# Kernel optimization log

Hardware: AMD Instinct MI355X
Metric: run time of the kernel (lower is better)

## Reference

```python
import jax, jax.numpy as jnp
import numpy as np

N = 2_097_152
TABLE = 32768  # hash table size (power of 2 -> mod == & 32767)
FEAT = 16
H = 64


def setup_inputs() -> dict:
    key = jax.random.key(0)
    k = jax.random.split(key, 9)
    pos = jax.random.normal(k[0], (N, 3), dtype=jnp.float32)
    normal = jax.random.normal(k[1], (N, 3), dtype=jnp.float32)
    emb = jax.random.normal(k[2], (TABLE, FEAT), dtype=jnp.float32) * 0.05
    W1 = jax.random.normal(k[3], (FEAT + 3, H), dtype=jnp.float32) * 0.1
    b1 = jnp.zeros((H,), jnp.float32)
    W2 = jax.random.normal(k[4], (H, H), dtype=jnp.float32) * 0.1
    b2 = jnp.zeros((H,), jnp.float32)
    W3 = jax.random.normal(k[5], (H, 3), dtype=jnp.float32) * 0.1
    b3 = jnp.zeros((3,), jnp.float32)
    return {"pos": pos, "normal": normal, "emb": emb,
            "W1": W1, "b1": b1, "W2": W2, "b2": b2, "W3": W3, "b3": b3}


def _hash_idx(pos):
    # torch .long() truncates toward zero; astype(int32) does the same.
    # Products only matter mod 2^15, so int32 wraparound is safe.
    s = (pos * 8.0).astype(jnp.int32)
    h = (s[:, 0] * np.int32(73856093)) ^ (s[:, 1] * np.int32(19349663)) ^ (s[:, 2] * np.int32(83492791))
    return h & np.int32(TABLE - 1)  # floor-mod by 2^15 == bitwise AND


def reference(pos, normal, emb, W1, b1, W2, b2, W3, b3):
    idx = _hash_idx(pos)                    # [N] int32
    feat = emb[idx]                         # [N,16] gather
    x = jnp.concatenate([feat, normal], axis=-1)  # [N,19]
    h1 = jax.nn.relu(x @ W1 + b1)           # [N,64]
    h2 = jax.nn.relu(h1 @ W2 + b2)          # [N,64]
    return jax.nn.sigmoid(h2 @ W3 + b3)     # [N,3]
```

## Files before the change

kernel.cpp:

```cpp
#include <hip/hip_runtime.h>
#include <cstdint>


typedef short  bf16x8 __attribute__((ext_vector_type(8)));
typedef float  f32x4  __attribute__((ext_vector_type(4)));

#define MFMA16(A, B, C) __builtin_amdgcn_mfma_f32_16x16x32_bf16((A), (B), (C), 0, 0, 0)

__device__ inline uint32_t f2b_u(float f) {
    union { float f; uint32_t u; } x; x.f = f;
    return (x.u + 0x7FFFu + ((x.u >> 16) & 1u)) >> 16;
}
__device__ inline short f2b(float f) { return (short)f2b_u(f); }

#if defined(__has_builtin)
#  if __has_builtin(__builtin_amdgcn_cvt_pk_bf16_f32)
#    define HAVE_PK_BF16 1
#  endif
#endif

__device__ inline int pk(float a, float b) {
#ifdef HAVE_PK_BF16
    auto v = __builtin_amdgcn_cvt_pk_bf16_f32(a, b);
    int i; __builtin_memcpy(&i, &v, sizeof(i));
    return i;
#else
    return (int)(f2b_u(a) | (f2b_u(b) << 16));
#endif
}

__device__ inline void cfence() { __asm__ volatile("" ::: "memory"); }

__device__ inline float sigmoid_fast(float x) {
    float e = __expf(-x);
    return __builtin_amdgcn_rcpf(1.0f + e);
}

#define XS 40
#define HS 72

__global__ __launch_bounds__(256, 3) void nrad_mfma_kernel(
    const float* __restrict__ pos, const float* __restrict__ nrm,
    const float* __restrict__ emb,
    const float* __restrict__ W1, const float* __restrict__ b1,
    const float* __restrict__ W2, const float* __restrict__ b2,
    const float* __restrict__ W3, const float* __restrict__ b3,
    float* __restrict__ out, int ntiles)
{
    __shared__ alignas(16) char arena[29696];
    short* w1t = (short*)arena;
    short* w2t = (short*)(arena + 4096);
    short* w3t = (short*)(arena + 12288);
    float* b2s = (float*)(arena + 12672);
    float* b3s = (float*)(arena + 12928);

    const int tid  = threadIdx.x;
    const int wave = tid >> 6;
    const int lane = tid & 63;
    const int q    = lane >> 4;
    const int nn   = lane & 15;

    for (int e = tid; e < 64 * 32; e += 256) {
        int n = e >> 5, k = e & 31;
        float v = (k < 19) ? W1[k * 64 + n] : (k == 19 ? b1[n] : 0.0f);
        w1t[n * 32 + k] = f2b(v);
    }
    for (int e = tid; e < 4096; e += 256) {
        int k = e >> 6, n = e & 63;
        w2t[n * 64 + k] = f2b(W2[e]);
    }
    for (int e = tid; e < 192; e += 256) {
        int k = e / 3, c = e - k * 3;
        w3t[c * 64 + k] = f2b(W3[e]);
    }
    for (int e = tid; e < 64; e += 256) b2s[e] = b2[e];
    if (tid < 4) b3s[tid] = (tid < 3) ? b3[tid] : 0.0f;
    __syncthreads();

    bf16x8 w1f[4], w2f[4][2], w3f[2];
    #pragma unroll
    for (int t = 0; t < 4; ++t)
        w1f[t] = *(const bf16x8*)(w1t + (t * 16 + nn) * 32 + q * 8);
    #pragma unroll
    for (int t = 0; t < 4; ++t)
        #pragma unroll
        for (int ks = 0; ks < 2; ++ks)
            w2f[t][ks] = *(const bf16x8*)(w2t + (t * 16 + nn) * 64 + ks * 32 + q * 8);
    {
        int c3 = (nn < 3) ? nn : 0;
        w3f[0] = *(const bf16x8*)(w3t + c3 * 64 + q * 8);
        w3f[1] = *(const bf16x8*)(w3t + c3 * 64 + 32 + q * 8);
    }
    f32x4 b2rv[4];
    #pragma unroll
    for (int t = 0; t < 4; ++t)
        b2rv[t] = *(const f32x4*)(b2s + t * 16 + q * 4);
    const float b3r = (nn < 3) ? b3s[nn] : 0.0f;
    __syncthreads();

    short* xw = (short*)(arena + wave * 5120);
    short* hw = (short*)(arena + 20480 + wave * 2304);

    const int xro  = nn * XS + q * 8;
    const int hro0 = nn * HS + q * 8;
    const int oofs = q * 12 + nn;

    const int wave_gid = blockIdx.x * 4 + wave;
    const int nwaves   = gridDim.x * 4;
    const float4* emb4 = (const float4*)emb;

    for (int tile = wave_gid; tile < ntiles; tile += nwaves) {
        const int base = tile * 64;
        const int i    = base + lane;

        const float* pp = pos + 3 * i;
        const float* np = nrm + 3 * i;
        float p0 = pp[0], p1 = pp[1], p2 = pp[2];
        float n0 = np[0], n1 = np[1], n2 = np[2];
        int s0 = (int)(p0 * 8.0f), s1 = (int)(p1 * 8.0f), s2 = (int)(p2 * 8.0f);
        uint32_t h = ((uint32_t)s0 * 73856093u) ^ ((uint32_t)s1 * 19349663u) ^
                     ((uint32_t)s2 * 83492791u);
        uint32_t idx = h & 32767u;
        float4 f0 = emb4[idx*4+0], f1 = emb4[idx*4+1];
        float4 f2 = emb4[idx*4+2], f3 = emb4[idx*4+3];

        int4 A = make_int4(pk(f0.x, f0.y), pk(f0.z, f0.w), pk(f1.x, f1.y), pk(f1.z, f1.w));
        int4 B = make_int4(pk(f2.x, f2.y), pk(f2.z, f2.w), pk(f3.x, f3.y), pk(f3.z, f3.w));
        int4 C = make_int4(pk(n0, n1), pk(n2, 1.0f), 0, 0);
        int4 D = make_int4(0, 0, 0, 0);
        int4* xr = (int4*)(xw + lane * XS);
        xr[0] = A; xr[1] = B; xr[2] = C; xr[3] = D;
        cfence();

        const float* ob = out + (size_t)base * 3;

        #pragma unroll
        for (int sub = 0; sub < 4; ++sub) {
            bf16x8 xf = *(const bf16x8*)(xw + sub * 16 * XS + xro);
            f32x4 acc1[4];
            #pragma unroll
            for (int t = 0; t < 4; ++t) {
                f32x4 z = {0.0f, 0.0f, 0.0f, 0.0f};
                acc1[t] = MFMA16(w1f[t], xf, z);
            }
            cfence();
            #pragma unroll
            for (int t = 0; t < 4; ++t) {
                float a0 = fmaxf(acc1[t][0], 0.0f), a1 = fmaxf(acc1[t][1], 0.0f);
                float a2 = fmaxf(acc1[t][2], 0.0f), a3 = fmaxf(acc1[t][3], 0.0f);
                *(int2*)(hw + nn * HS + t * 16 + q * 4) = make_int2(pk(a0, a1), pk(a2, a3));
            }
            cfence();

            bf16x8 h1f0 = *(const bf16x8*)(hw + hro0);
            bf16x8 h1f1 = *(const bf16x8*)(hw + hro0 + 32);
            f32x4 acc2[4];
            #pragma unroll
            for (int t = 0; t < 4; ++t) {
                f32x4 c2 = b2rv[t];
                c2 = MFMA16(w2f[t][0], h1f0, c2);
                acc2[t] = MFMA16(w2f[t][1], h1f1, c2);
            }
            cfence();
            #pragma unroll
            for (int t = 0; t < 4; ++t) {
                float a0 = fmaxf(acc2[t][0], 0.0f), a1 = fmaxf(acc2[t][1], 0.0f);
                float a2 = fmaxf(acc2[t][2], 0.0f), a3 = fmaxf(acc2[t][3], 0.0f);
                *(int2*)(hw + nn * HS + t * 16 + q * 4) = make_int2(pk(a0, a1), pk(a2, a3));
            }
            cfence();

            bf16x8 h2f0 = *(const bf16x8*)(hw + hro0);
            bf16x8 h2f1 = *(const bf16x8*)(hw + hro0 + 32);
            f32x4 acc3 = {b3r, b3r, b3r, b3r};
            acc3 = MFMA16(h2f0, w3f[0], acc3);
            acc3 = MFMA16(h2f1, w3f[1], acc3);
            cfence();

            float o0 = sigmoid_fast(acc3[0]);
            float o1 = sigmoid_fast(acc3[1]);
            float o2 = sigmoid_fast(acc3[2]);
            float o3 = sigmoid_fast(acc3[3]);
            if (nn < 3) {
                const float* dummy = ob;  (void)dummy;
                float* o = (float*)(ob + sub * 48 + oofs);
                o[0] = o0; o[3] = o1; o[6] = o2; o[9] = o3;
            }
        }
        cfence();
    }
}

extern "C" void kernel_launch(void* const* d_in, const int* in_sizes, int n_in,
                              void* d_out, int out_size, void* d_ws, size_t ws_size,
                              hipStream_t stream) {
    const float* pos = (const float*)d_in[0];
    const float* nrm = (const float*)d_in[1];
    const float* emb = (const float*)d_in[2];
    const float* W1  = (const float*)d_in[3];
    const float* b1  = (const float*)d_in[4];
    const float* W2  = (const float*)d_in[5];
    const float* b2  = (const float*)d_in[6];
    const float* W3  = (const float*)d_in[7];
    const float* b3  = (const float*)d_in[8];
    float* out = (float*)d_out;

    int n = in_sizes[0] / 3;
    int ntiles = n / 64;
    int grid = 1024;
    nrad_mfma_kernel<<<grid, 256, 0, stream>>>(pos, nrm, emb, W1, b1, W2, b2,
                                               W3, b3, out, ntiles);
}
```

Baseline: 165.8 us.

## Convert MFMA outputs to next-layer operands with permlane swaps instead of LDS

Replaces the per-layer LDS round trip (store the packed bf16 activations, then reload them as B-operand fragments) with in-register packing followed by v_permlane32_swap and v_permlane16_swap, which move the accumulator layout into the operand layout directly. This drops the hw LDS scratch, shrinking shared memory to 20 KB, and raises launch bounds to four blocks per CU. It also forces the inline-asm v_cvt_pk_bf16_f32 packing path. The risks are the correctness of the lane-permutation mapping and extra register pressure under the tighter occupancy bound.

```diff
diff --git a/kernel.cpp b/kernel.cpp
--- a/kernel.cpp
+++ b/kernel.cpp
@@ -7,26 +7,22 @@
 
 #define MFMA16(A, B, C) __builtin_amdgcn_mfma_f32_16x16x32_bf16((A), (B), (C), 0, 0, 0)
 
+__device__ inline int pk(float a, float b) {
+    int d;
+    __asm__("v_cvt_pk_bf16_f32 %0, %1, %2" : "=v"(d) : "v"(a), "v"(b));
+    return d;
+}
 __device__ inline uint32_t f2b_u(float f) {
     union { float f; uint32_t u; } x; x.f = f;
     return (x.u + 0x7FFFu + ((x.u >> 16) & 1u)) >> 16;
 }
 __device__ inline short f2b(float f) { return (short)f2b_u(f); }
 
-#if defined(__has_builtin)
-#  if __has_builtin(__builtin_amdgcn_cvt_pk_bf16_f32)
-#    define HAVE_PK_BF16 1
-#  endif
-#endif
-
-__device__ inline int pk(float a, float b) {
-#ifdef HAVE_PK_BF16
-    auto v = __builtin_amdgcn_cvt_pk_bf16_f32(a, b);
-    int i; __builtin_memcpy(&i, &v, sizeof(i));
-    return i;
-#else
-    return (int)(f2b_u(a) | (f2b_u(b) << 16));
-#endif
+__device__ inline void pl32_swap(int& a, int& b) {
+    __asm__ volatile("v_permlane32_swap_b32 %0, %1" : "+v"(a), "+v"(b));
+}
+__device__ inline void pl16_swap(int& a, int& b) {
+    __asm__ volatile("v_permlane16_swap_b32 %0, %1" : "+v"(a), "+v"(b));
 }
 
 __device__ inline void cfence() { __asm__ volatile("" ::: "memory"); }
@@ -36,10 +32,30 @@
     return __builtin_amdgcn_rcpf(1.0f + e);
 }
 
+__device__ inline void cd_to_frag(const f32x4 acc[4], int4& lo, int4& hi) {
+    int P0 = pk(fmaxf(acc[0][0],0.f), fmaxf(acc[0][1],0.f));
+    int P1 = pk(fmaxf(acc[0][2],0.f), fmaxf(acc[0][3],0.f));
+    int P2 = pk(fmaxf(acc[1][0],0.f), fmaxf(acc[1][1],0.f));
+    int P3 = pk(fmaxf(acc[1][2],0.f), fmaxf(acc[1][3],0.f));
+    int P4 = pk(fmaxf(acc[2][0],0.f), fmaxf(acc[2][1],0.f));
+    int P5 = pk(fmaxf(acc[2][2],0.f), fmaxf(acc[2][3],0.f));
+    int P6 = pk(fmaxf(acc[3][0],0.f), fmaxf(acc[3][1],0.f));
+    int P7 = pk(fmaxf(acc[3][2],0.f), fmaxf(acc[3][3],0.f));
+    pl32_swap(P0, P2); pl16_swap(P0, P2);
+    pl32_swap(P1, P3); pl16_swap(P1, P3);
+    pl32_swap(P4, P6); pl16_swap(P4, P6);
+    pl32_swap(P5, P7); pl16_swap(P5, P7);
+    lo = make_int4(P0, P1, P2, P3);
+    hi = make_int4(P4, P5, P6, P7);
+}
+
+__device__ inline bf16x8 as_frag(int4 v) {
+    bf16x8 f; __builtin_memcpy(&f, &v, sizeof(f)); return f;
+}
+
 #define XS 40
-#define HS 72
-
-__global__ __launch_bounds__(256, 3) void nrad_mfma_kernel(
+
+__global__ __launch_bounds__(256, 4) void nrad_mfma_kernel(
     const float* __restrict__ pos, const float* __restrict__ nrm,
     const float* __restrict__ emb,
     const float* __restrict__ W1, const float* __restrict__ b1,
@@ -47,7 +63,7 @@
     const float* __restrict__ W3, const float* __restrict__ b3,
     float* __restrict__ out, int ntiles)
 {
-    __shared__ alignas(16) char arena[29696];
+    __shared__ alignas(16) char arena[20480];
     short* w1t = (short*)arena;
     short* w2t = (short*)(arena + 4096);
     short* w3t = (short*)(arena + 12288);
@@ -99,10 +115,8 @@
     __syncthreads();
 
     short* xw = (short*)(arena + wave * 5120);
-    short* hw = (short*)(arena + 20480 + wave * 2304);
 
     const int xro  = nn * XS + q * 8;
-    const int hro0 = nn * HS + q * 8;
     const int oofs = q * 12 + nn;
 
     const int wave_gid = blockIdx.x * 4 + wave;
@@ -143,46 +157,31 @@
                 f32x4 z = {0.0f, 0.0f, 0.0f, 0.0f};
                 acc1[t] = MFMA16(w1f[t], xf, z);
             }
-            cfence();
-            #pragma unroll
-            for (int t = 0; t < 4; ++t) {
-                float a0 = fmaxf(acc1[t][0], 0.0f), a1 = fmaxf(acc1[t][1], 0.0f);
-                float a2 = fmaxf(acc1[t][2], 0.0f), a3 = fmaxf(acc1[t][3], 0.0f);
-                *(int2*)(hw + nn * HS + t * 16 + q * 4) = make_int2(pk(a0, a1), pk(a2, a3));
-            }
-            cfence();
-
-            bf16x8 h1f0 = *(const bf16x8*)(hw + hro0);
-            bf16x8 h1f1 = *(const bf16x8*)(hw + hro0 + 32);
+
+            int4 h1lo, h1hi;
+            cd_to_frag(acc1, h1lo, h1hi);
+            bf16x8 h1f0 = as_frag(h1lo), h1f1 = as_frag(h1hi);
+
             f32x4 acc2[4];
             #pragma unroll
             for (int t = 0; t < 4; ++t) {
-                f32x4 c2 = b2rv[t];
-                c2 = MFMA16(w2f[t][0], h1f0, c2);
-                acc2[t] = MFMA16(w2f[t][1], h1f1, c2);
+                f32x4 c2 = MFMA16(w2f[t][0], h1f0, b2rv[t]);
+                acc2[t]  = MFMA16(w2f[t][1], h1f1, c2);
             }
-            cfence();
-            #pragma unroll
-            for (int t = 0; t < 4; ++t) {
-                float a0 = fmaxf(acc2[t][0], 0.0f), a1 = fmaxf(acc2[t][1], 0.0f);
-                float a2 = fmaxf(acc2[t][2], 0.0f), a3 = fmaxf(acc2[t][3], 0.0f);
-                *(int2*)(hw + nn * HS + t * 16 + q * 4) = make_int2(pk(a0, a1), pk(a2, a3));
-            }
-            cfence();
-
-            bf16x8 h2f0 = *(const bf16x8*)(hw + hro0);
-            bf16x8 h2f1 = *(const bf16x8*)(hw + hro0 + 32);
-            f32x4 acc3 = {b3r, b3r, b3r, b3r};
-            acc3 = MFMA16(h2f0, w3f[0], acc3);
-            acc3 = MFMA16(h2f1, w3f[1], acc3);
-            cfence();
+
+            int4 h2lo, h2hi;
+            cd_to_frag(acc2, h2lo, h2hi);
+            bf16x8 h2f0 = as_frag(h2lo), h2f1 = as_frag(h2hi);
+
+            f32x4 cb = {b3r, b3r, b3r, b3r};
+            f32x4 c3a = MFMA16(h2f0, w3f[0], cb);
+            f32x4 acc3 = MFMA16(h2f1, w3f[1], c3a);
 
             float o0 = sigmoid_fast(acc3[0]);
             float o1 = sigmoid_fast(acc3[1]);
             float o2 = sigmoid_fast(acc3[2]);
             float o3 = sigmoid_fast(acc3[3]);
             if (nn < 3) {
-                const float* dummy = ob;  (void)dummy;
                 float* o = (float*)(ob + sub * 48 + oofs);
                 o[0] = o0; o[3] = o1; o[6] = o2; o[9] = o3;
             }
```

New measurement: 152.1 us. -8.2%, faster.
